# Kernel tuning notes

Hardware: AMD Instinct MI355X
Metric: run time of the kernel (lower is better)

## Reference

```python
import jax, jax.numpy as jnp
import numpy as np

DIM = 1024
HEADS = 16
HEAD_DIM = DIM // HEADS
B, S, L0, L1 = 2, 2048, 2048, 2048


def setup_inputs() -> dict:
    key = jax.random.key(0)
    ks = jax.random.split(key, 10)
    sc = DIM ** -0.5
    return {
        "query": jax.random.normal(ks[0], (B, S, DIM), jnp.float32),
        "l0_keys": jax.random.normal(ks[1], (B, L0, DIM), jnp.float32),
        "l0_values": jax.random.normal(ks[2], (B, L0, DIM), jnp.float32),
        "l1_keys": jax.random.normal(ks[3], (B, L1, DIM), jnp.float32),
        "l1_values": jax.random.normal(ks[4], (B, L1, DIM), jnp.float32),
        "l0_mask": jax.random.randint(ks[5], (S, L0), 0, 2, jnp.int32),
        "Wq": jax.random.normal(ks[6], (DIM, DIM), jnp.float32) * sc,
        "bq": jnp.zeros((DIM,), jnp.float32),
        "Wo": jax.random.normal(ks[7], (DIM, DIM), jnp.float32) * sc,
        "bo": jnp.zeros((DIM,), jnp.float32),
        "gate": jnp.asarray(0.0, jnp.float32),
    }


def reference(query, l0_keys, l0_values, l1_keys, l1_values, l0_mask, Wq, bq, Wo, bo, gate):
    b, s, d = query.shape
    h, hd = HEADS, HEAD_DIM
    scale = hd ** -0.5
    # q: [B,H,S,hd]
    q = (query @ Wq.T + bq).reshape(b, s, h, hd).transpose(0, 2, 1, 3)

    def attend(keys, values, mask):
        L = keys.shape[1]
        k = keys.reshape(b, L, h, hd)
        v = values.reshape(b, L, h, hd)
        scores = jnp.einsum("bhsd,blhd->bhsl", q, k) * scale
        if mask is not None:
            scores = jnp.where(mask[None, None] == 0, -jnp.inf, scores)
        w = jax.nn.softmax(scores, axis=-1)  # [B,H,S,L]
        out = jnp.einsum("bhsl,blhd->bshd", w, v)  # [B,S,H,hd]
        return out, w.mean(axis=1)

    out0, a0 = attend(l0_keys, l0_values, l0_mask)
    out1, a1 = attend(l1_keys, l1_values, None)
    g = jax.nn.sigmoid(gate)
    out = (g * out0 + (1.0 - g) * out1).reshape(b, s, d)
    out = out @ Wo.T + bo
    return out, a0, a1
```

## Files before the change

kernel.cpp:

```cpp
#include <hip/hip_runtime.h>

#define DIM   1024
#define HEADS 16
#define HD    64
#define BB    2
#define SS    2048
#define LLL   2048
#define LOG2E 1.4426950408889634f

typedef __bf16 bf16x8 __attribute__((ext_vector_type(8)));
typedef __bf16 bf16x4v __attribute__((ext_vector_type(4)));
typedef float  f32x4  __attribute__((ext_vector_type(4)));
typedef short  s16x4  __attribute__((ext_vector_type(4)));
typedef unsigned short u16;

static __device__ __forceinline__ u16 f2b(float x) {
  unsigned u = __float_as_uint(x);
  u += 0x7fffu + ((u >> 16) & 1u);
  return (u16)(u >> 16);
}
static __device__ __forceinline__ float b2f(u16 u) {
  return __uint_as_float(((unsigned)u) << 16);
}
static __device__ __forceinline__ f32x4 mfma32(bf16x8 a, bf16x8 b, f32x4 c) {
  return __builtin_amdgcn_mfma_f32_16x16x32_bf16(a, b, c, 0, 0, 0);
}

static __device__ __forceinline__ void gload_lds16(const void* g, void* lds_uniform_base) {
#if __has_builtin(__builtin_amdgcn_global_load_lds)
  __builtin_amdgcn_global_load_lds(
      (const __attribute__((address_space(1))) unsigned int*)g,
      (__attribute__((address_space(3))) unsigned int*)lds_uniform_base, 16, 0, 0);
#else
  const int l = threadIdx.x & 63;
  ((uint4*)lds_uniform_base)[l] = ((const uint4*)g)[0];
#endif
}

__global__ void cvt3(const float* __restrict__ a, const float* __restrict__ b,
                     const float* __restrict__ c, u16* __restrict__ da,
                     u16* __restrict__ db_, u16* __restrict__ dc, int na4, int nb4) {
  int i = blockIdx.x * blockDim.x + threadIdx.x;
  const float* s; u16* d; int j = i;
  if (j < na4) { s = a; d = da; }
  else if ((j -= na4) < nb4) { s = b; d = db_; }
  else { j -= nb4; s = c; d = dc; }
  float4 f = ((const float4*)s)[j];
  ushort4 o;
  o.x = f2b(f.x); o.y = f2b(f.y); o.z = f2b(f.z); o.w = f2b(f.w);
  ((ushort4*)d)[j] = o;
}

__global__ void mask_pack(const int* __restrict__ mask, unsigned* __restrict__ mbits) {
  int i = blockIdx.x * blockDim.x + threadIdx.x;
  const int* src = mask + (size_t)i * 32;
  unsigned bm = 0;
#pragma unroll
  for (int j = 0; j < 8; ++j) {
    int4 m = ((const int4*)src)[j];
    bm |= (m.x != 0 ? 1u : 0u) << (j * 4 + 0);
    bm |= (m.y != 0 ? 1u : 0u) << (j * 4 + 1);
    bm |= (m.z != 0 ? 1u : 0u) << (j * 4 + 2);
    bm |= (m.w != 0 ? 1u : 0u) << (j * 4 + 3);
  }
  mbits[i] = bm;
}

__global__ __launch_bounds__(256) void pack_k(const float* __restrict__ k0,
                                              const float* __restrict__ k1,
                                              u16* __restrict__ Kfrag) {
  const float SCK = 0.125f * LOG2E;
  const int w = threadIdx.x >> 6, l = threadIdx.x & 63, g = l >> 4, li = l & 15;
  const int lt = blockIdx.x * 4 + w, h = blockIdx.y, z = blockIdx.z;
  const int lay = z >> 1, b = z & 1;
  const float* src = (lay ? k1 : k0) + (size_t)b * LLL * DIM;
  u16* dst = Kfrag + ((((size_t)z * HEADS + h) * 32 + lt) * 8) * 512;
#pragma unroll
  for (int c = 0; c < 8; ++c) {
    int mt = c >> 1, kk = c & 1;
    const float* p = &src[(size_t)(lt * 64 + mt * 16 + li) * DIM + h * 64 + kk * 32 + g * 8];
    float4 f0 = *(const float4*)p;
    float4 f1 = *(const float4*)(p + 4);
    u16 u[8] = {f2b(f0.x * SCK), f2b(f0.y * SCK), f2b(f0.z * SCK), f2b(f0.w * SCK),
                f2b(f1.x * SCK), f2b(f1.y * SCK), f2b(f1.z * SCK), f2b(f1.w * SCK)};
    *(uint4*)&dst[c * 512 + l * 8] = *(uint4*)u;
  }
}

__global__ __launch_bounds__(256) void pack_v(const float* __restrict__ v0,
                                              const float* __restrict__ v1,
                                              u16* __restrict__ Vfrag) {
  __shared__ u16 T[64][72];
  const int lt = blockIdx.x, h = blockIdx.y, z = blockIdx.z;
  const int lay = z >> 1, b = z & 1;
  const float* v = (lay ? v1 : v0) + (size_t)b * LLL * DIM;
  const int t = threadIdx.x;
  {
    int r = t >> 2, c16 = (t & 3) * 16;
    const float* src = &v[(size_t)(lt * 64 + r) * DIM + h * 64 + c16];
#pragma unroll
    for (int i = 0; i < 4; ++i) {
      float4 f = *(const float4*)&src[i * 4];
      T[r][c16 + i * 4 + 0] = f2b(f.x);
      T[r][c16 + i * 4 + 1] = f2b(f.y);
      T[r][c16 + i * 4 + 2] = f2b(f.z);
      T[r][c16 + i * 4 + 3] = f2b(f.w);
    }
  }
  __syncthreads();
  u16* dst = Vfrag + ((((size_t)z * HEADS + h) * 32 + lt) * 8) * 512;
  {
    int lane = t & 63, g = lane >> 4, li = lane & 15;
#pragma unroll
    for (int cc = 0; cc < 2; ++cc) {
      int c = (t >> 6) + cc * 4;
      int pair = c >> 2, dt = c & 3;
      u16 u[8];
#pragma unroll
      for (int j = 0; j < 4; ++j) u[j]     = T[pair * 32 + 4 * g + j][dt * 16 + li];
#pragma unroll
      for (int j = 0; j < 4; ++j) u[4 + j] = T[pair * 32 + 16 + 4 * g + j][dt * 16 + li];
      *(uint4*)&dst[c * 512 + lane * 8] = *(uint4*)u;
    }
  }
}

template<int MODE>
__global__ __launch_bounds__(256) void gemm_nt(const u16* __restrict__ A,
                                               const u16* __restrict__ Bt,
                                               const float* __restrict__ bias,
                                               void* __restrict__ Cv,
                                               int M, int N, int K) {
  __shared__ u16 As[2][128][64];
  __shared__ u16 Bs[2][64][64];
  const int t = threadIdx.x;
  const int w = t >> 6, l = t & 63, g = l >> 4, li = l & 15;
  const int m0 = blockIdx.y * 128, n0 = blockIdx.x * 64;
  const int slotL = w * 64 + l;
  const int rA = slotL >> 3, cA = ((slotL & 7) * 8) ^ ((rA & 7) * 8);

  auto stageAB = [&](int buf, int kt) {
#pragma unroll
    for (int s = 0; s < 4; ++s) {
      int r = rA + s * 32;
      gload_lds16(&A[(size_t)(m0 + r) * K + kt + cA], &As[buf][0][0] + (s * 256 + w * 64) * 8);
    }
#pragma unroll
    for (int s = 0; s < 2; ++s) {
      int r = rA + s * 32;
      gload_lds16(&Bt[(size_t)(n0 + r) * K + kt + cA], &Bs[buf][0][0] + (s * 256 + w * 64) * 8);
    }
  };

  f32x4 acc[2][4] = {};
  stageAB(0, 0);
  __syncthreads();
  int cur = 0;
  for (int kt = 0; kt < K; kt += 64) {
    if (kt + 64 < K) stageAB(cur ^ 1, kt + 64);
#pragma unroll
    for (int kk = 0; kk < 2; ++kk) {
      bf16x8 a[2], bfr[4];
#pragma unroll
      for (int mi = 0; mi < 2; ++mi) {
        int ra = w * 32 + mi * 16 + li;
        a[mi] = *(const bf16x8*)&As[cur][ra][(kk * 32 + g * 8) ^ ((ra & 7) << 3)];
      }
#pragma unroll
      for (int ni = 0; ni < 4; ++ni) {
        int rb = ni * 16 + li;
        bfr[ni] = *(const bf16x8*)&Bs[cur][rb][(kk * 32 + g * 8) ^ ((rb & 7) << 3)];
      }
#pragma unroll
      for (int mi = 0; mi < 2; ++mi)
#pragma unroll
        for (int ni = 0; ni < 4; ++ni)
          acc[mi][ni] = mfma32(a[mi], bfr[ni], acc[mi][ni]);
    }
    __syncthreads();
    cur ^= 1;
  }
#pragma unroll
  for (int mi = 0; mi < 2; ++mi)
#pragma unroll
    for (int ni = 0; ni < 4; ++ni)
#pragma unroll
      for (int v = 0; v < 4; ++v) {
        int rr = m0 + w * 32 + mi * 16 + g * 4 + v;
        int cc = n0 + ni * 16 + li;
        float val = acc[mi][ni][v] + bias[cc];
        if (MODE == 1) {
          ((float*)Cv)[(size_t)rr * N + cc] = val;
        } else {
          int b = rr >> 11, q = rr & 2047;
          int qt = q >> 5, n = (q >> 4) & 1, liq = q & 15;
          int h = (cc >> 6) & 15, kk2 = (cc >> 5) & 1, gp = (cc >> 3) & 3, j = cc & 7;
          size_t base = ((((size_t)b * HEADS + h) * 64 + qt) * 4 + n * 2 + kk2) * 512;
          ((u16*)Cv)[base + (size_t)(gp * 16 + liq) * 8 + j] = f2b(val);
        }
      }
}

template<int MASKED>
static __device__ __forceinline__ void attn_pv_body(int z, int h, int qt, int w, int l,
                                                    const u16* __restrict__ Qfrag,
                                                    const u16* __restrict__ Kfrag,
                                                    const u16* __restrict__ Vfrag,
                                                    const unsigned* __restrict__ mbits,
                                                    u16* __restrict__ out01,
                                                    float* __restrict__ db,
                                                    u16* __restrict__ KV) {
  const int g = l >> 4, li = l & 15;
  const int b = z & 1;
  const u16* kfh = Kfrag + (size_t)(z * HEADS + h) * (32 * 8 * 512);
  const u16* vfh = Vfrag + (size_t)(z * HEADS + h) * (32 * 8 * 512);
  const u16* qfh = Qfrag + (((size_t)(b * HEADS + h) * 64 + qt) * 4) * 512;

  bf16x8 qf[2][2];
#pragma unroll
  for (int n = 0; n < 2; ++n)
#pragma unroll
    for (int kk = 0; kk < 2; ++kk)
      qf[n][kk] = *(const bf16x8*)&qfh[(n * 2 + kk) * 512 + l * 8];

  const unsigned* mrow0 = MASKED ? mbits + (size_t)(qt * 32 + li) * (LLL / 32) : nullptr;
  const unsigned* mrow1 = MASKED ? mrow0 + 16 * (LLL / 32) : nullptr;
  const int shb = 4 * g;
  bf16x8 ones8;
#pragma unroll
  for (int j = 0; j < 8; ++j) ones8[j] = __builtin_bit_cast(__bf16, (u16)0x3F80);

  auto stage = [&](int buf, int lt) {
    const u16* kfl = kfh + (size_t)lt * 4096;
    const u16* vfl = vfh + (size_t)lt * 4096;
#pragma unroll
    for (int i2 = 0; i2 < 2; ++i2) {
      int f = w * 2 + i2;
      const u16* gsrc = (f < 8 ? kfl + f * 512 : vfl + (f - 8) * 512) + l * 8;
      gload_lds16(gsrc, (char*)KV + buf * 16384 + f * 1024);
    }
  };

  f32x4 dacc[2] = {};
  f32x4 oacc[4][2] = {};

  stage(0, 0);
  __syncthreads();
  int cur = 0;
  for (int lt = 0; lt < 32; ++lt) {
    if (lt + 1 < 32) stage(cur ^ 1, lt + 1);
    unsigned mw[2][2];
    if (MASKED) {
      mw[0][0] = mrow0[lt * 2]; mw[0][1] = mrow0[lt * 2 + 1];
      mw[1][0] = mrow1[lt * 2]; mw[1][1] = mrow1[lt * 2 + 1];
    }
    const u16* Ks = KV + cur * 8192;
    const u16* Vs = Ks + 4096;

    auto qk = [&](f32x4 (&s)[2], int mt) {
      bf16x8 k0 = *(const bf16x8*)&Ks[(mt * 2 + 0) * 512 + l * 8];
      bf16x8 k1 = *(const bf16x8*)&Ks[(mt * 2 + 1) * 512 + l * 8];
      f32x4 zz = {};
      __builtin_amdgcn_s_setprio(1);
      s[0] = mfma32(k0, qf[0][0], zz);
      s[0] = mfma32(k1, qf[0][1], s[0]);
      s[1] = mfma32(k0, qf[1][0], zz);
      s[1] = mfma32(k1, qf[1][1], s[1]);
      __builtin_amdgcn_s_setprio(0);
    };
    auto sm = [&](f32x4 (&s)[2], int mt, s16x4 (&wpk)[2]) {
#pragma unroll
      for (int n = 0; n < 2; ++n) {
        unsigned mm = MASKED ? (mw[n][mt >> 1] >> ((mt & 1) * 16 + shb)) : 0u;
        f32x4 ev;
#pragma unroll
        for (int v = 0; v < 4; ++v) {
          float e = __builtin_amdgcn_exp2f(s[n][v]);
          if (MASKED) {
            int spread = ((int)(mm << (31 - v))) >> 31;
            e = __uint_as_float(__float_as_uint(e) & (unsigned)spread);
          }
          ev[v] = e;
        }
        bf16x4v wb = __builtin_convertvector(ev, bf16x4v);
        wpk[n] = __builtin_bit_cast(s16x4, wb);
      }
    };
    auto pv_pair = [&](s16x4 (&w0)[2], s16x4 (&w1)[2], int pair) {
      bf16x8 w8[2];
#pragma unroll
      for (int n = 0; n < 2; ++n) {
        bf16x4v a0 = __builtin_bit_cast(bf16x4v, w0[n]);
        bf16x4v a1 = __builtin_bit_cast(bf16x4v, w1[n]);
        w8[n] = __builtin_shufflevector(a0, a1, 0, 1, 2, 3, 4, 5, 6, 7);
      }
      __builtin_amdgcn_s_setprio(1);
      dacc[0] = mfma32(ones8, w8[0], dacc[0]);
      dacc[1] = mfma32(ones8, w8[1], dacc[1]);
#pragma unroll
      for (int dt = 0; dt < 4; ++dt) {
        bf16x8 vf = *(const bf16x8*)&Vs[(pair * 4 + dt) * 512 + l * 8];
#pragma unroll
        for (int n = 0; n < 2; ++n)
          oacc[dt][n] = mfma32(vf, w8[n], oacc[dt][n]);
      }
      __builtin_amdgcn_s_setprio(0);
    };

    f32x4 sA[2], sB[2];
    s16x4 wA[2], wB[2];
    qk(sA, 0); qk(sB, 1);
    sm(sA, 0, wA);
    qk(sA, 2);
    sm(sB, 1, wB);
    pv_pair(wA, wB, 0);
    qk(sB, 3);
    sm(sA, 2, wA);
    sm(sB, 3, wB);
    pv_pair(wA, wB, 1);
    __syncthreads();
    cur ^= 1;
  }
  float dinv[2];
  dinv[0] = 1.0f / dacc[0][0];
  dinv[1] = 1.0f / dacc[1][0];
  if (l < 16) {
    db[(size_t)(z * HEADS + h) * SS + qt * 32 + li]      = -__log2f(dacc[0][0]);
    db[(size_t)(z * HEADS + h) * SS + qt * 32 + 16 + li] = -__log2f(dacc[1][0]);
  }
  u16* ob = out01 + (size_t)z * SS * DIM;
#pragma unroll
  for (int dt = 0; dt < 4; ++dt)
#pragma unroll
    for (int n = 0; n < 2; ++n) {
      f32x4 o = oacc[dt][n] * dinv[n];
      ushort4 us;
      us.x = f2b(o[0]); us.y = f2b(o[1]); us.z = f2b(o[2]); us.w = f2b(o[3]);
      *(ushort4*)&ob[((size_t)(qt * 32 + n * 16 + li)) * DIM + h * HD + dt * 16 + 4 * g] = us;
    }
}

__global__ __launch_bounds__(512, 4) void attn_pv(const u16* __restrict__ Qfrag,
                                                  const u16* __restrict__ Kfrag,
                                                  const u16* __restrict__ Vfrag,
                                                  const unsigned* __restrict__ mbits,
                                                  u16* __restrict__ out01,
                                                  float* __restrict__ db) {
  __shared__ u16 KV[2][8192];
  const int flat = blockIdx.x;
  const int xcd = flat & 7, i = flat >> 3;
  const int k = i >> 3, qg = i & 7;
  const int zh = xcd + 8 * k;
  const int z = zh >> 4, h = zh & 15;
  const int w = threadIdx.x >> 6, l = threadIdx.x & 63;
  const int qt = qg * 8 + w;
  if (z < 2) attn_pv_body<1>(z, h, qt, w, l, Qfrag, Kfrag, Vfrag, mbits, out01, db, &KV[0][0]);
  else       attn_pv_body<0>(z, h, qt, w, l, Qfrag, Kfrag, Vfrag, mbits, out01, db, &KV[0][0]);
}

template<int MASKED>
static __device__ __forceinline__ void amean_body(int z, int qt, int lt, int w, int l,
                                                  const u16* __restrict__ Qfrag,
                                                  const u16* __restrict__ Kfrag,
                                                  const unsigned* __restrict__ mbits,
                                                  const float* __restrict__ db,
                                                  float* __restrict__ aout,
                                                  u16* __restrict__ KS) {
  const int g = l >> 4, li = l & 15;
  const int b = z & 1;

  unsigned mw[2][2];
  if (MASKED) {
    const unsigned* m0 = mbits + (size_t)(qt * 32 + li) * (LLL / 32) + lt * 2;
    const unsigned* m1 = m0 + 16 * (LLL / 32);
    mw[0][0] = m0[0]; mw[0][1] = m0[1];
    mw[1][0] = m1[0]; mw[1][1] = m1[1];
  }
  const u16* qf_base = Qfrag + (((size_t)(b * HEADS) * 64 + qt) * 4) * 512 + l * 8;
  const float* dbb = db + (size_t)(z * HEADS) * SS + qt * 32 + li;

  auto stageK = [&](int buf, int h) {
    const u16* kfh = Kfrag + ((((size_t)(z * HEADS + h)) * 32 + lt) * 8) * 512;
#pragma unroll
    for (int i2 = 0; i2 < 2; ++i2) {
      int f = w * 2 + i2;
      gload_lds16(kfh + f * 512 + l * 8, (char*)KS + buf * 8192 + f * 1024);
    }
  };

  f32x4 asum[4][2] = {};
  stageK(0, 0);
  __syncthreads();
#pragma unroll 2
  for (int h = 0; h < HEADS; ++h) {
    if (h + 1 < HEADS) stageK((h + 1) & 1, h + 1);
    float l2[2];
    l2[0] = dbb[(size_t)h * SS];
    l2[1] = dbb[(size_t)h * SS + 16];
    bf16x8 qf[2][2];
#pragma unroll
    for (int n = 0; n < 2; ++n)
#pragma unroll
      for (int kk = 0; kk < 2; ++kk)
        qf[n][kk] = *(const bf16x8*)&qf_base[(size_t)h * (64 * 4 * 512) + (n * 2 + kk) * 512];
    const u16* Ks = KS + (h & 1) * 4096;
#pragma unroll
    for (int mt = 0; mt < 4; ++mt) {
      bf16x8 k0 = *(const bf16x8*)&Ks[(mt * 2 + 0) * 512 + l * 8];
      bf16x8 k1 = *(const bf16x8*)&Ks[(mt * 2 + 1) * 512 + l * 8];
#pragma unroll
      for (int n = 0; n < 2; ++n) {
        f32x4 s = {};
        s = mfma32(k0, qf[n][0], s);
        s = mfma32(k1, qf[n][1], s);
        unsigned mm = MASKED ? (mw[n][mt >> 1] >> ((mt & 1) * 16 + 4 * g)) : 0u;
#pragma unroll
        for (int v = 0; v < 4; ++v) {
          float e = __builtin_amdgcn_exp2f(s[v] + l2[n]);
          if (MASKED) {
            int spread = ((int)(mm << (31 - v))) >> 31;
            e = __uint_as_float(__float_as_uint(e) & (unsigned)spread);
          }
          asum[mt][n][v] += e;
        }
      }
    }
    __syncthreads();
  }
  float* ab = aout + (size_t)z * SS * LLL;
#pragma unroll
  for (int mt = 0; mt < 4; ++mt)
#pragma unroll
    for (int n = 0; n < 2; ++n) {
      f32x4 o = asum[mt][n] * 0.0625f;
      f32x4* dst = (f32x4*)&ab[(size_t)(qt * 32 + n * 16 + li) * LLL + lt * 64 + mt * 16 + 4 * g];
      __builtin_nontemporal_store(o, dst);
    }
}

__global__ __launch_bounds__(256, 4) void amean(const u16* __restrict__ Qfrag,
                                                const u16* __restrict__ Kfrag,
                                                const unsigned* __restrict__ mbits,
                                                const float* __restrict__ db,
                                                float* __restrict__ aout) {
  __shared__ u16 KS[2][4096];
  const int flat = blockIdx.x;
  const int xcd = flat & 7, i = flat >> 3;
  const int k = i >> 4, qg = i & 15;
  const int zlt = xcd + 8 * k;
  const int z = zlt >> 5, lt = zlt & 31;
  const int w = threadIdx.x >> 6, l = threadIdx.x & 63;
  const int qt = qg * 4 + w;
  if (z < 2) amean_body<1>(z, qt, lt, w, l, Qfrag, Kfrag, mbits, db, aout, &KS[0][0]);
  else       amean_body<0>(z, qt, lt, w, l, Qfrag, Kfrag, mbits, db, aout, &KS[0][0]);
}

__global__ void merge_kernel(const u16* __restrict__ o01,
                             const float* __restrict__ gate,
                             u16* __restrict__ merged) {
  int i = blockIdx.x * blockDim.x + threadIdx.x;
  float gv = gate[0];
  float g = 1.0f / (1.0f + __builtin_amdgcn_exp2f(-gv * LOG2E));
  const size_t n = (size_t)BB * SS * DIM;
  ushort4 a = ((const ushort4*)o01)[i];
  ushort4 c = ((const ushort4*)(o01 + n))[i];
  ushort4 o;
  o.x = f2b(g * b2f(a.x) + (1.f - g) * b2f(c.x));
  o.y = f2b(g * b2f(a.y) + (1.f - g) * b2f(c.y));
  o.z = f2b(g * b2f(a.z) + (1.f - g) * b2f(c.z));
  o.w = f2b(g * b2f(a.w) + (1.f - g) * b2f(c.w));
  ((ushort4*)merged)[i] = o;
}

extern "C" void kernel_launch(void* const* d_in, const int* in_sizes, int n_in,
                              void* d_out, int out_size, void* d_ws, size_t ws_size,
                              hipStream_t stream) {
  const float* query = (const float*)d_in[0];
  const float* k0f   = (const float*)d_in[1];
  const float* v0f   = (const float*)d_in[2];
  const float* k1f   = (const float*)d_in[3];
  const float* v1f   = (const float*)d_in[4];
  const int*   mask  = (const int*)d_in[5];
  const float* Wqf   = (const float*)d_in[6];
  const float* bq    = (const float*)d_in[7];
  const float* Wof   = (const float*)d_in[8];
  const float* bo    = (const float*)d_in[9];
  const float* gate  = (const float*)d_in[10];
  float* out = (float*)d_out;

  const size_t nQ = (size_t)BB * SS * DIM;
  const size_t nW = (size_t)DIM * DIM;

  char* ws = (char*)d_ws;
  size_t off = 0;
  auto alloc = [&](size_t bytes) -> char* {
    char* p = ws + off;
    off += (bytes + 255) & ~(size_t)255;
    return p;
  };
  u16*      queryb  = (u16*)alloc(nQ * 2);
  u16*      wqb     = (u16*)alloc(nW * 2);
  u16*      wob     = (u16*)alloc(nW * 2);
  u16*      Qfrag   = (u16*)alloc(nQ * 2);
  u16*      Kfrag   = (u16*)alloc((size_t)2 * nQ * 2);
  u16*      Vfrag   = (u16*)alloc((size_t)2 * nQ * 2);
  unsigned* mbits   = (unsigned*)alloc((size_t)SS * (LLL / 32) * 4);
  float*    db      = (float*)alloc((size_t)4 * HEADS * SS * 4);
  u16*      out01   = (u16*)alloc((size_t)2 * nQ * 2);
  u16*      mergedb = queryb;

  {
    int na4 = (int)(nQ / 4), nb4 = (int)(nW / 4);
    int tot = na4 + 2 * nb4;
    cvt3<<<dim3(tot / 256), dim3(256), 0, stream>>>(query, Wqf, Wof, queryb, wqb, wob, na4, nb4);
  }

  mask_pack<<<dim3(SS * (LLL / 32) / 256), dim3(256), 0, stream>>>(mask, mbits);
  pack_k<<<dim3(LLL / 64 / 4, HEADS, 4), dim3(256), 0, stream>>>(k0f, k1f, Kfrag);
  pack_v<<<dim3(LLL / 64, HEADS, 4), dim3(256), 0, stream>>>(v0f, v1f, Vfrag);

  gemm_nt<2><<<dim3(DIM / 64, (BB * SS) / 128), dim3(256), 0, stream>>>(
      queryb, wqb, bq, (void*)Qfrag, BB * SS, DIM, DIM);

  attn_pv<<<dim3(512), dim3(512), 0, stream>>>(Qfrag, Kfrag, Vfrag, mbits, out01, db);

  amean<<<dim3(2048), dim3(256), 0, stream>>>(Qfrag, Kfrag, mbits, db, out + nQ);

  merge_kernel<<<dim3((int)(nQ / 4 / 256)), dim3(256), 0, stream>>>(out01, gate, mergedb);

  gemm_nt<1><<<dim3(DIM / 64, (BB * SS) / 128), dim3(256), 0, stream>>>(
      mergedb, wob, bo, (void*)out, BB * SS, DIM, DIM);
}
```

Measured before the change: 207.8 us.

## Widen amean blocks to 8 waves, fuse mask packing into convert kernel

The amean kernel now runs 512-thread blocks with 8 waves sharing each staged K tile, so every wave issues one LDS-bound load instead of two. This halves the block count and doubles reuse of each K tile across query tiles. MFMA issue is wrapped in s_setprio to favour matrix instructions. The mask bit-packing kernel is folded into the bf16 conversion kernel to save a launch. The larger blocks may reduce occupancy under the same register budget.

```diff
diff --git a/kernel.cpp b/kernel.cpp
--- a/kernel.cpp
+++ b/kernel.cpp
@@ -37,33 +37,35 @@
 #endif
 }
 
-__global__ void cvt3(const float* __restrict__ a, const float* __restrict__ b,
+__global__ void prep(const float* __restrict__ a, const float* __restrict__ b,
                      const float* __restrict__ c, u16* __restrict__ da,
-                     u16* __restrict__ db_, u16* __restrict__ dc, int na4, int nb4) {
+                     u16* __restrict__ db_, u16* __restrict__ dc,
+                     const int* __restrict__ mask, unsigned* __restrict__ mbits,
+                     int na4, int nb4, int ncvt) {
   int i = blockIdx.x * blockDim.x + threadIdx.x;
-  const float* s; u16* d; int j = i;
-  if (j < na4) { s = a; d = da; }
-  else if ((j -= na4) < nb4) { s = b; d = db_; }
-  else { j -= nb4; s = c; d = dc; }
-  float4 f = ((const float4*)s)[j];
-  ushort4 o;
-  o.x = f2b(f.x); o.y = f2b(f.y); o.z = f2b(f.z); o.w = f2b(f.w);
-  ((ushort4*)d)[j] = o;
-}
-
-__global__ void mask_pack(const int* __restrict__ mask, unsigned* __restrict__ mbits) {
-  int i = blockIdx.x * blockDim.x + threadIdx.x;
-  const int* src = mask + (size_t)i * 32;
-  unsigned bm = 0;
-#pragma unroll
-  for (int j = 0; j < 8; ++j) {
-    int4 m = ((const int4*)src)[j];
-    bm |= (m.x != 0 ? 1u : 0u) << (j * 4 + 0);
-    bm |= (m.y != 0 ? 1u : 0u) << (j * 4 + 1);
-    bm |= (m.z != 0 ? 1u : 0u) << (j * 4 + 2);
-    bm |= (m.w != 0 ? 1u : 0u) << (j * 4 + 3);
-  }
-  mbits[i] = bm;
+  if (i < ncvt) {
+    const float* s; u16* d; int j = i;
+    if (j < na4) { s = a; d = da; }
+    else if ((j -= na4) < nb4) { s = b; d = db_; }
+    else { j -= nb4; s = c; d = dc; }
+    float4 f = ((const float4*)s)[j];
+    ushort4 o;
+    o.x = f2b(f.x); o.y = f2b(f.y); o.z = f2b(f.z); o.w = f2b(f.w);
+    ((ushort4*)d)[j] = o;
+  } else {
+    int j = i - ncvt;
+    const int* src = mask + (size_t)j * 32;
+    unsigned bm = 0;
+#pragma unroll
+    for (int jj = 0; jj < 8; ++jj) {
+      int4 m = ((const int4*)src)[jj];
+      bm |= (m.x != 0 ? 1u : 0u) << (jj * 4 + 0);
+      bm |= (m.y != 0 ? 1u : 0u) << (jj * 4 + 1);
+      bm |= (m.z != 0 ? 1u : 0u) << (jj * 4 + 2);
+      bm |= (m.w != 0 ? 1u : 0u) << (jj * 4 + 3);
+    }
+    mbits[j] = bm;
+  }
 }
 
 __global__ __launch_bounds__(256) void pack_k(const float* __restrict__ k0,
@@ -381,11 +383,7 @@
 
   auto stageK = [&](int buf, int h) {
     const u16* kfh = Kfrag + ((((size_t)(z * HEADS + h)) * 32 + lt) * 8) * 512;
-#pragma unroll
-    for (int i2 = 0; i2 < 2; ++i2) {
-      int f = w * 2 + i2;
-      gload_lds16(kfh + f * 512 + l * 8, (char*)KS + buf * 8192 + f * 1024);
-    }
+    gload_lds16(kfh + w * 512 + l * 8, (char*)KS + buf * 8192 + w * 1024);
   };
 
   f32x4 asum[4][2] = {};
@@ -410,9 +408,12 @@
       bf16x8 k1 = *(const bf16x8*)&Ks[(mt * 2 + 1) * 512 + l * 8];
 #pragma unroll
       for (int n = 0; n < 2; ++n) {
-        f32x4 s = {};
-        s = mfma32(k0, qf[n][0], s);
+        f32x4 s;
+        __builtin_amdgcn_s_setprio(1);
+        f32x4 zz = {};
+        s = mfma32(k0, qf[n][0], zz);
         s = mfma32(k1, qf[n][1], s);
+        __builtin_amdgcn_s_setprio(0);
         unsigned mm = MASKED ? (mw[n][mt >> 1] >> ((mt & 1) * 16 + 4 * g)) : 0u;
 #pragma unroll
         for (int v = 0; v < 4; ++v) {
@@ -438,7 +439,7 @@
     }
 }
 
-__global__ __launch_bounds__(256, 4) void amean(const u16* __restrict__ Qfrag,
+__global__ __launch_bounds__(512, 4) void amean(const u16* __restrict__ Qfrag,
                                                 const u16* __restrict__ Kfrag,
                                                 const unsigned* __restrict__ mbits,
                                                 const float* __restrict__ db,
@@ -446,11 +447,11 @@
   __shared__ u16 KS[2][4096];
   const int flat = blockIdx.x;
   const int xcd = flat & 7, i = flat >> 3;
-  const int k = i >> 4, qg = i & 15;
+  const int k = i >> 3, qg = i & 7;
   const int zlt = xcd + 8 * k;
   const int z = zlt >> 5, lt = zlt & 31;
   const int w = threadIdx.x >> 6, l = threadIdx.x & 63;
-  const int qt = qg * 4 + w;
+  const int qt = qg * 8 + w;
   if (z < 2) amean_body<1>(z, qt, lt, w, l, Qfrag, Kfrag, mbits, db, aout, &KS[0][0]);
   else       amean_body<0>(z, qt, lt, w, l, Qfrag, Kfrag, mbits, db, aout, &KS[0][0]);
 }
@@ -511,11 +512,12 @@
 
   {
     int na4 = (int)(nQ / 4), nb4 = (int)(nW / 4);
-    int tot = na4 + 2 * nb4;
-    cvt3<<<dim3(tot / 256), dim3(256), 0, stream>>>(query, Wqf, Wof, queryb, wqb, wob, na4, nb4);
-  }
-
-  mask_pack<<<dim3(SS * (LLL / 32) / 256), dim3(256), 0, stream>>>(mask, mbits);
+    int ncvt = na4 + 2 * nb4;
+    int nmask = SS * (LLL / 32);
+    prep<<<dim3((ncvt + nmask) / 256), dim3(256), 0, stream>>>(
+        query, Wqf, Wof, queryb, wqb, wob, mask, mbits, na4, nb4, ncvt);
+  }
+
   pack_k<<<dim3(LLL / 64 / 4, HEADS, 4), dim3(256), 0, stream>>>(k0f, k1f, Kfrag);
   pack_v<<<dim3(LLL / 64, HEADS, 4), dim3(256), 0, stream>>>(v0f, v1f, Vfrag);
 
@@ -524,7 +526,7 @@
 
   attn_pv<<<dim3(512), dim3(512), 0, stream>>>(Qfrag, Kfrag, Vfrag, mbits, out01, db);
 
-  amean<<<dim3(2048), dim3(256), 0, stream>>>(Qfrag, Kfrag, mbits, db, out + nQ);
+  amean<<<dim3(1024), dim3(512), 0, stream>>>(Qfrag, Kfrag, mbits, db, out + nQ);
 
   merge_kernel<<<dim3((int)(nQ / 4 / 256)), dim3(256), 0, stream>>>(out01, gate, mergedb);
 
```

New measurement: 213.1 us. 2.5% more time.
